# Kernel optimization log

Hardware: AMD Instinct MI355X
Metric: run time of the kernel (lower is better)

The kernel has to match this reference:

```python
import jax, jax.numpy as jnp
import numpy as np

N_NODES = 100000
N_EDGES = 1600000
IN_DIM = 128
HID_DIM = 128
OUT_DIM = 16
N_GRAPHS = 128


def setup_inputs() -> dict:
    key = jax.random.key(0)
    ks = jax.random.split(key, 8)
    x = jax.random.normal(ks[0], (N_NODES, IN_DIM), dtype=jnp.float32)
    edge_index = jax.random.randint(ks[1], (2, N_EDGES), 0, N_NODES, dtype=jnp.int64)
    batch = jnp.sort(jax.random.randint(ks[2], (N_NODES,), 0, N_GRAPHS, dtype=jnp.int64))
    # GCNConv params (glorot-ish scale) and Linear params
    w1 = jax.random.normal(ks[3], (IN_DIM, HID_DIM), dtype=jnp.float32) / np.sqrt(IN_DIM)
    b1 = jnp.zeros((HID_DIM,), dtype=jnp.float32)
    w2 = jax.random.normal(ks[4], (HID_DIM, HID_DIM), dtype=jnp.float32) / np.sqrt(HID_DIM)
    b2 = jnp.zeros((HID_DIM,), dtype=jnp.float32)
    wc = jax.random.normal(ks[5], (HID_DIM, OUT_DIM), dtype=jnp.float32) / np.sqrt(HID_DIM)
    bc = jnp.zeros((OUT_DIM,), dtype=jnp.float32)
    return {"x": x, "edge_index": edge_index, "batch": batch,
            "w1": w1, "b1": b1, "w2": w2, "b2": b2, "wc": wc, "bc": bc}


def _gcn_layer(h, src, dst, w, b, n_nodes):
    # h: [N, Fin]; src/dst: [E+N] (self-loops already appended)
    h = h @ w  # [N, Fout]
    ones = jnp.ones_like(dst, dtype=h.dtype)
    deg = jax.ops.segment_sum(ones, dst, num_segments=n_nodes)  # [N]
    dinv = jnp.where(deg > 0, jax.lax.rsqrt(deg), 0.0)
    norm = dinv[src] * dinv[dst]  # [E+N]
    msg = h[src] * norm[:, None]  # gather + scale, [E+N, Fout]
    out = jax.ops.segment_sum(msg, dst, num_segments=n_nodes)  # scatter-add
    return out + b


def reference(x, edge_index, batch, w1, b1, w2, b2, wc, bc):
    n = x.shape[0]
    loop = jnp.arange(n, dtype=edge_index.dtype)
    src = jnp.concatenate([edge_index[0], loop])  # add self-loops (PyG default)
    dst = jnp.concatenate([edge_index[1], loop])

    h = jax.nn.relu(_gcn_layer(x, src, dst, w1, b1, n))
    h = jax.nn.relu(_gcn_layer(h, src, dst, w2, b2, n))

    # global mean pool over graphs
    sums = jax.ops.segment_sum(h, batch, num_segments=N_GRAPHS)  # [G, H]
    cnt = jax.ops.segment_sum(jnp.ones((n,), h.dtype), batch, num_segments=N_GRAPHS)
    pooled = sums / jnp.maximum(cnt, 1.0)[:, None]

    return pooled @ wc + bc  # [G, OUT_DIM]
```

## Files before the change

kernel.cpp:

```cpp
#include <hip/hip_runtime.h>
#include <stdint.h>

#define NN 100000
#define NE 1600000
#define FDIM 128
#define NGRAPH 128
#define ODIM 16
#define NBKT 391
#define CAP 4608
#define SCHUNK 8192
#define NSCAT ((NE + SCHUNK - 1) / SCHUNK)
#define NSTARTB ((NN + 255) / 256)

typedef __attribute__((ext_vector_type(8))) short short8;
typedef __attribute__((ext_vector_type(8))) unsigned short ushort8;
typedef __attribute__((ext_vector_type(4))) float f32x4;

__device__ __forceinline__ float blo(unsigned int p) { return __uint_as_float(p << 16); }
__device__ __forceinline__ float bhi(unsigned int p) { return __uint_as_float(p & 0xffff0000u); }
__device__ __forceinline__ unsigned short f2b(float f) {
    unsigned int u = __float_as_uint(f);
    unsigned int r = (u + 0x7fffu + ((u >> 16) & 1u)) >> 16;
    return (unsigned short)r;
}
__device__ __forceinline__ unsigned int packbf(float lo, float hi) {
    return (unsigned int)f2b(lo) | ((unsigned int)f2b(hi) << 16);
}

__device__ __forceinline__ int detect_w(const int* __restrict__ ei) {
    int lane = threadIdx.x & 63;
    int v = ei[2 * lane + 1];
    return (__ballot(v != 0) == 0ULL) ? 1 : 0;
}
__device__ __forceinline__ int ld_idx(const int* __restrict__ p, long long i, int w) {
    return w ? p[2 * i] : p[i];
}

__global__ void __launch_bounds__(256) k_prep(
    const float* __restrict__ w1, const float* __restrict__ w2,
    unsigned short* __restrict__ wt1, unsigned short* __restrict__ wt2,
    const int* __restrict__ ei, const int* __restrict__ batch,
    int* __restrict__ gstart, int* __restrict__ bcursor,
    unsigned short* __restrict__ xws)
{
    int b = blockIdx.x, t = threadIdx.x;
    if (b < 128) {
        int idx = b * 256 + t;
        int which = idx >> 14, r = idx & 16383;
        int k = r >> 7, j = r & 127;
        const float* w = which ? w2 : w1;
        unsigned short* wt = which ? wt2 : wt1;
        wt[j * 128 + k] = f2b(w[k * 128 + j]);
    } else if (b < 128 + NSTARTB) {
        int w = detect_w(ei);
        int i = (b - 128) * 256 + t;
        if (i < NN) {
            int bb = ld_idx(batch, i, w);
            int prev = (i == 0) ? -1 : ld_idx(batch, i - 1, w);
            for (int g = prev + 1; g <= bb; ++g) gstart[g] = i;
            if (i == NN - 1)
                for (int g = bb + 1; g <= NGRAPH; ++g) gstart[g] = NN;
        }
    } else {
        int i = (b - 128 - NSTARTB) * 256 + t;
        if (i < NBKT) bcursor[i] = i * CAP;
        if (b == 128 + NSTARTB && t < FDIM) xws[(size_t)NN * FDIM + t] = 0;
    }
}

__global__ void __launch_bounds__(512) k_scat(const int* __restrict__ ei,
                                              int* __restrict__ bcursor,
                                              unsigned int* __restrict__ rec) {
    __shared__ int hist[NBKT];
    __shared__ int gbase[NBKT];
    __shared__ int lcur[NBKT];
    int t = threadIdx.x;
    int w = detect_w(ei);
    for (int i = t; i < NBKT; i += 512) hist[i] = 0;
    __syncthreads();
    long long e0 = (long long)blockIdx.x * SCHUNK;
    unsigned int myrec[16];
    int mybkt[16];
    #pragma unroll
    for (int j = 0; j < 16; ++j) {
        long long e = e0 + j * 512 + t;
        if (e < NE) {
            int s = ld_idx(ei, e, w);
            int d = ld_idx(ei, NE + e, w);
            mybkt[j] = d >> 8;
            myrec[j] = (unsigned int)s | ((unsigned int)(d & 255) << 17);
            atomicAdd(&hist[mybkt[j]], 1);
        } else mybkt[j] = -1;
    }
    __syncthreads();
    for (int i = t; i < NBKT; i += 512) {
        int c = hist[i];
        gbase[i] = c ? atomicAdd(&bcursor[i], c) : 0;
        lcur[i] = 0;
    }
    __syncthreads();
    #pragma unroll
    for (int j = 0; j < 16; ++j) {
        int b = mybkt[j];
        if (b >= 0) {
            int r = atomicAdd(&lcur[b], 1);
            int p = gbase[b] + r;
            if (p < (b + 1) * CAP) rec[p] = myrec[j];
        }
    }
}

__global__ void __launch_bounds__(256) k_bucket(const unsigned int* __restrict__ rec,
                                                const int* __restrict__ bcursor,
                                                int* __restrict__ csr,
                                                int* __restrict__ offs,
                                                int* __restrict__ deg,
                                                float* __restrict__ dinv) {
    __shared__ unsigned int rbuf[CAP];
    __shared__ int srcout[CAP];
    __shared__ int hist[256], scn[256], cur[256];
    int b = blockIdx.x, t = threadIdx.x;
    int base = b * CAP;
    int cnt = bcursor[b] - base;
    if (cnt > CAP) cnt = CAP;
    hist[t] = 0;
    __syncthreads();
    for (int j = t; j < cnt; j += 256) {
        unsigned int r = rec[base + j];
        rbuf[j] = r;
        atomicAdd(&hist[r >> 17], 1);
    }
    __syncthreads();
    int v = hist[t];
    scn[t] = v;
    __syncthreads();
    for (int o = 1; o < 256; o <<= 1) {
        int tv = (t >= o) ? scn[t - o] : 0;
        __syncthreads();
        scn[t] += tv;
        __syncthreads();
    }
    int excl = scn[t] - v;
    cur[t] = excl;
    int node = (b << 8) + t;
    if (node < NN) {
        offs[node] = base + excl;
        deg[node] = v;
        dinv[node] = rsqrtf((float)(v + 1));
    }
    __syncthreads();
    for (int j = t; j < cnt; j += 256) {
        unsigned int r = rbuf[j];
        int p = atomicAdd(&cur[r >> 17], 1);
        srcout[p] = (int)(r & 0x1FFFFu);
    }
    __syncthreads();
    for (int j = t; j < cnt; j += 256) csr[base + j] = srcout[j];
}

#define LWS 136
template <bool BF16IN>
__global__ void __launch_bounds__(256) k_gemm(
    const void* __restrict__ Xv,
    const unsigned short* __restrict__ WT,
    const float* __restrict__ dinv,
    unsigned short* __restrict__ OUT)
{
    __shared__ unsigned short lw[128 * LWS];
    int tid = threadIdx.x;
    for (int it = 0; it < 8; ++it) {
        int vidx = it * 256 + tid;
        int j = vidx >> 4, kc = vidx & 15;
        ushort8 v = *(const ushort8*)(WT + j * 128 + kc * 8);
        *(ushort8*)(&lw[j * LWS + kc * 8]) = v;
    }
    __syncthreads();

    int wave = tid >> 6, lane = tid & 63;
    int quad = lane >> 4, n16 = lane & 15;
    int row0 = (blockIdx.x * 4 + wave) * 16;
    if (row0 >= NN) return;

    f32x4 acc[8];
    for (int ct = 0; ct < 8; ++ct) acc[ct] = (f32x4){0.f, 0.f, 0.f, 0.f};

    const int arow = row0 + n16;
    for (int kk = 0; kk < 4; ++kk) {
        short8 a;
        if (BF16IN) {
            a = *(const short8*)((const unsigned short*)Xv + (size_t)arow * 128 + kk * 32 + quad * 8);
        } else {
            const float* ap = (const float*)Xv + (size_t)arow * 128 + kk * 32 + quad * 8;
            float4 a01 = *(const float4*)(ap);
            float4 a23 = *(const float4*)(ap + 4);
            a[0] = (short)f2b(a01.x); a[1] = (short)f2b(a01.y);
            a[2] = (short)f2b(a01.z); a[3] = (short)f2b(a01.w);
            a[4] = (short)f2b(a23.x); a[5] = (short)f2b(a23.y);
            a[6] = (short)f2b(a23.z); a[7] = (short)f2b(a23.w);
        }
        for (int ct = 0; ct < 8; ++ct) {
            short8 b = *(const short8*)(&lw[(ct * 16 + n16) * LWS + kk * 32 + quad * 8]);
            acc[ct] = __builtin_amdgcn_mfma_f32_16x16x32_bf16(a, b, acc[ct], 0, 0, 0);
        }
    }
    for (int r = 0; r < 4; ++r) {
        int row = row0 + quad * 4 + r;
        float dv = dinv[row];
        for (int ct = 0; ct < 8; ++ct)
            OUT[(size_t)row * 128 + ct * 16 + n16] = f2b(acc[ct][r] * dv);
    }
}

__global__ void __launch_bounds__(256) k_agg(
    const unsigned short* __restrict__ XWS,
    const int* __restrict__ csr,
    const int* __restrict__ offs,
    const int* __restrict__ deg,
    const float* __restrict__ dinv,
    const float* __restrict__ bias,
    unsigned short* __restrict__ H)
{
    int wave = threadIdx.x >> 6, lane = threadIdx.x & 63;
    int v = blockIdx.x * 4 + wave;
    int g = lane >> 4, f = lane & 15;
    int beg = offs[v], end = beg + deg[v];
    float a[8];
    {
        uint4 q = *(const uint4*)(XWS + (size_t)v * FDIM + f * 8);
        float m = (g == 0) ? 1.f : 0.f;
        a[0] = m * blo(q.x); a[1] = m * bhi(q.x); a[2] = m * blo(q.y); a[3] = m * bhi(q.y);
        a[4] = m * blo(q.z); a[5] = m * bhi(q.z); a[6] = m * blo(q.w); a[7] = m * bhi(q.w);
    }
    int e1 = end - 1;
    for (int j = beg; j < end; j += 16) {
        int j0 = j + g, j1 = j + 4 + g, j2 = j + 8 + g, j3 = j + 12 + g;
        int i0 = csr[j0 < end ? j0 : e1]; i0 = (j0 < end) ? i0 : NN;
        int i1 = csr[j1 < end ? j1 : e1]; i1 = (j1 < end) ? i1 : NN;
        int i2 = csr[j2 < end ? j2 : e1]; i2 = (j2 < end) ? i2 : NN;
        int i3 = csr[j3 < end ? j3 : e1]; i3 = (j3 < end) ? i3 : NN;
        uint4 q0 = *(const uint4*)(XWS + (size_t)i0 * FDIM + f * 8);
        uint4 q1 = *(const uint4*)(XWS + (size_t)i1 * FDIM + f * 8);
        uint4 q2 = *(const uint4*)(XWS + (size_t)i2 * FDIM + f * 8);
        uint4 q3 = *(const uint4*)(XWS + (size_t)i3 * FDIM + f * 8);
        a[0] += blo(q0.x); a[1] += bhi(q0.x); a[2] += blo(q0.y); a[3] += bhi(q0.y);
        a[4] += blo(q0.z); a[5] += bhi(q0.z); a[6] += blo(q0.w); a[7] += bhi(q0.w);
        a[0] += blo(q1.x); a[1] += bhi(q1.x); a[2] += blo(q1.y); a[3] += bhi(q1.y);
        a[4] += blo(q1.z); a[5] += bhi(q1.z); a[6] += blo(q1.w); a[7] += bhi(q1.w);
        a[0] += blo(q2.x); a[1] += bhi(q2.x); a[2] += blo(q2.y); a[3] += bhi(q2.y);
        a[4] += blo(q2.z); a[5] += bhi(q2.z); a[6] += blo(q2.w); a[7] += bhi(q2.w);
        a[0] += blo(q3.x); a[1] += bhi(q3.x); a[2] += blo(q3.y); a[3] += bhi(q3.y);
        a[4] += blo(q3.z); a[5] += bhi(q3.z); a[6] += blo(q3.w); a[7] += bhi(q3.w);
    }
    #pragma unroll
    for (int i = 0; i < 8; ++i) {
        a[i] += __shfl_xor(a[i], 16);
        a[i] += __shfl_xor(a[i], 32);
    }
    if (g == 0) {
        float dv = dinv[v];
        float4 b0 = *(const float4*)(bias + f * 8);
        float4 b1 = *(const float4*)(bias + f * 8 + 4);
        uint4 o;
        o.x = packbf(fmaxf(fmaf(a[0], dv, b0.x), 0.f), fmaxf(fmaf(a[1], dv, b0.y), 0.f));
        o.y = packbf(fmaxf(fmaf(a[2], dv, b0.z), 0.f), fmaxf(fmaf(a[3], dv, b0.w), 0.f));
        o.z = packbf(fmaxf(fmaf(a[4], dv, b1.x), 0.f), fmaxf(fmaf(a[5], dv, b1.y), 0.f));
        o.w = packbf(fmaxf(fmaf(a[6], dv, b1.z), 0.f), fmaxf(fmaf(a[7], dv, b1.w), 0.f));
        *(uint4*)(H + (size_t)v * FDIM + f * 8) = o;
    }
}

__global__ void __launch_bounds__(256) k_poolcls(
    const unsigned short* __restrict__ H, const int* __restrict__ gstart,
    const float* __restrict__ wc, const float* __restrict__ bc,
    float* __restrict__ out)
{
    __shared__ float red[512];
    __shared__ float pl[FDIM];
    int g = blockIdx.x;
    int t = threadIdx.x;
    int pair = t & 63;
    int seg = t >> 6;
    int beg = gstart[g], end = gstart[g + 1];
    float a0 = 0.f, a1 = 0.f;
    for (int i = beg + seg; i < end; i += 4) {
        unsigned int q = *(const unsigned int*)(H + (size_t)i * FDIM + 2 * pair);
        a0 += blo(q); a1 += bhi(q);
    }
    red[t] = a0; red[256 + t] = a1;
    __syncthreads();
    if (seg == 0) {
        a0 = red[t] + red[t + 64] + red[t + 128] + red[t + 192];
        a1 = red[256 + t] + red[256 + t + 64] + red[256 + t + 128] + red[256 + t + 192];
        float inv = 1.f / fmaxf((float)(end - beg), 1.f);
        pl[2 * pair] = a0 * inv;
        pl[2 * pair + 1] = a1 * inv;
    }
    __syncthreads();
    int o = t & 15, fs = t >> 4;
    float acc = 0.f;
    #pragma unroll
    for (int k = 0; k < 8; ++k)
        acc += pl[fs * 8 + k] * wc[(fs * 8 + k) * ODIM + o];
    red[t] = acc;
    __syncthreads();
    if (t < 16) {
        float s = bc[t];
        #pragma unroll
        for (int k = 0; k < 16; ++k) s += red[k * 16 + t];
        out[g * ODIM + t] = s;
    }
}

extern "C" void kernel_launch(void* const* d_in, const int* in_sizes, int n_in,
                              void* d_out, int out_size, void* d_ws, size_t ws_size,
                              hipStream_t stream) {
    const float* x   = (const float*)d_in[0];
    const int* ei    = (const int*)d_in[1];
    const int* batch = (const int*)d_in[2];
    const float* w1  = (const float*)d_in[3];
    const float* b1  = (const float*)d_in[4];
    const float* w2  = (const float*)d_in[5];
    const float* b2  = (const float*)d_in[6];
    const float* wc  = (const float*)d_in[7];
    const float* bc  = (const float*)d_in[8];
    float* out = (float*)d_out;

    char* ws = (char*)d_ws;
    size_t off = 0;
    auto alloc = [&](size_t bytes) -> void* {
        off = (off + 255) & ~(size_t)255;
        void* p = ws + off;
        off += bytes;
        return p;
    };
    int*   bcursor = (int*)alloc(NBKT * 4);
    int*   offs    = (int*)alloc(NN * 4);
    int*   deg     = (int*)alloc(NN * 4);
    float* dinv    = (float*)alloc(NN * 4);
    int*   gstart  = (int*)alloc((NGRAPH + 1) * 4);
    unsigned int* rec = (unsigned int*)alloc((size_t)NBKT * CAP * 4);
    int*   csr     = (int*)alloc((size_t)NBKT * CAP * 4 + 256);
    unsigned short* wt1 = (unsigned short*)alloc(128 * 128 * 2);
    unsigned short* wt2 = (unsigned short*)alloc(128 * 128 * 2);
    unsigned short* xws = (unsigned short*)alloc((size_t)(NN + 1) * FDIM * 2);
    unsigned short* h   = (unsigned short*)alloc((size_t)NN * FDIM * 2);

    k_prep<<<128 + NSTARTB + 2, 256, 0, stream>>>(w1, w2, wt1, wt2, ei, batch, gstart, bcursor, xws);
    k_scat<<<NSCAT, 512, 0, stream>>>(ei, bcursor, rec);
    k_bucket<<<NBKT, 256, 0, stream>>>(rec, bcursor, csr, offs, deg, dinv);

    k_gemm<false><<<(NN / 16 + 3) / 4, 256, 0, stream>>>(x, wt1, dinv, xws);
    k_agg<<<NN / 4, 256, 0, stream>>>(xws, csr, offs, deg, dinv, b1, h);
    k_gemm<true><<<(NN / 16 + 3) / 4, 256, 0, stream>>>(h, wt2, dinv, xws);
    k_agg<<<NN / 4, 256, 0, stream>>>(xws, csr, offs, deg, dinv, b2, h);
    k_poolcls<<<NGRAPH, 256, 0, stream>>>(h, gstart, wc, bc, out);
}
```

Baseline: 334.7 us.

## Fuse first-layer aggregation with second-layer GEMM into one kernel

Adds k_aggmm, which aggregates neighbor features for 16 nodes per block, applies bias, ReLU and dinv, stages the bf16 hidden rows in LDS, and multiplies them by W2 with MFMA before writing the scaled result. This removes the second k_gemm launch and the round trip of the hidden activation through global memory. In exchange each block loads the full W2 tile into LDS, and each wave serially aggregates 4 nodes, which lowers parallelism in the gather phase. k_prep is also launched a second time so the new xws2 buffer gets its padding row initialised.

```diff
diff --git a/kernel.cpp b/kernel.cpp
--- a/kernel.cpp
+++ b/kernel.cpp
@@ -159,9 +159,8 @@
 }
 
 #define LWS 136
-template <bool BF16IN>
 __global__ void __launch_bounds__(256) k_gemm(
-    const void* __restrict__ Xv,
+    const float* __restrict__ X,
     const unsigned short* __restrict__ WT,
     const float* __restrict__ dinv,
     unsigned short* __restrict__ OUT)
@@ -186,18 +185,14 @@
 
     const int arow = row0 + n16;
     for (int kk = 0; kk < 4; ++kk) {
+        const float* ap = X + (size_t)arow * 128 + kk * 32 + quad * 8;
+        float4 a01 = *(const float4*)(ap);
+        float4 a23 = *(const float4*)(ap + 4);
         short8 a;
-        if (BF16IN) {
-            a = *(const short8*)((const unsigned short*)Xv + (size_t)arow * 128 + kk * 32 + quad * 8);
-        } else {
-            const float* ap = (const float*)Xv + (size_t)arow * 128 + kk * 32 + quad * 8;
-            float4 a01 = *(const float4*)(ap);
-            float4 a23 = *(const float4*)(ap + 4);
-            a[0] = (short)f2b(a01.x); a[1] = (short)f2b(a01.y);
-            a[2] = (short)f2b(a01.z); a[3] = (short)f2b(a01.w);
-            a[4] = (short)f2b(a23.x); a[5] = (short)f2b(a23.y);
-            a[6] = (short)f2b(a23.z); a[7] = (short)f2b(a23.w);
-        }
+        a[0] = (short)f2b(a01.x); a[1] = (short)f2b(a01.y);
+        a[2] = (short)f2b(a01.z); a[3] = (short)f2b(a01.w);
+        a[4] = (short)f2b(a23.x); a[5] = (short)f2b(a23.y);
+        a[6] = (short)f2b(a23.z); a[7] = (short)f2b(a23.w);
         for (int ct = 0; ct < 8; ++ct) {
             short8 b = *(const short8*)(&lw[(ct * 16 + n16) * LWS + kk * 32 + quad * 8]);
             acc[ct] = __builtin_amdgcn_mfma_f32_16x16x32_bf16(a, b, acc[ct], 0, 0, 0);
@@ -208,6 +203,97 @@
         float dv = dinv[row];
         for (int ct = 0; ct < 8; ++ct)
             OUT[(size_t)row * 128 + ct * 16 + n16] = f2b(acc[ct][r] * dv);
+    }
+}
+
+__global__ void __launch_bounds__(256) k_aggmm(
+    const unsigned short* __restrict__ XWS,
+    const unsigned short* __restrict__ WT2,
+    const int* __restrict__ csr,
+    const int* __restrict__ offs,
+    const int* __restrict__ deg,
+    const float* __restrict__ dinv,
+    const float* __restrict__ bias,
+    unsigned short* __restrict__ OUT)
+{
+    __shared__ unsigned short lw[128 * LWS];
+    __shared__ unsigned short lh[16 * LWS];
+    int tid = threadIdx.x;
+    for (int it = 0; it < 8; ++it) {
+        int vidx = it * 256 + tid;
+        int j = vidx >> 4, kc = vidx & 15;
+        ushort8 v = *(const ushort8*)(WT2 + j * 128 + kc * 8);
+        *(ushort8*)(&lw[j * LWS + kc * 8]) = v;
+    }
+    int wave = tid >> 6, lane = tid & 63;
+    int g = lane >> 4, f = lane & 15;
+    int n0 = blockIdx.x * 16;
+
+    for (int nn = 0; nn < 4; ++nn) {
+        int v = n0 + wave * 4 + nn;
+        int beg = offs[v], end = beg + deg[v];
+        float a[8];
+        {
+            uint4 q = *(const uint4*)(XWS + (size_t)v * FDIM + f * 8);
+            float m = (g == 0) ? 1.f : 0.f;
+            a[0] = m * blo(q.x); a[1] = m * bhi(q.x); a[2] = m * blo(q.y); a[3] = m * bhi(q.y);
+            a[4] = m * blo(q.z); a[5] = m * bhi(q.z); a[6] = m * blo(q.w); a[7] = m * bhi(q.w);
+        }
+        int e1 = end - 1;
+        for (int j = beg; j < end; j += 16) {
+            int j0 = j + g, j1 = j + 4 + g, j2 = j + 8 + g, j3 = j + 12 + g;
+            int i0 = csr[j0 < end ? j0 : e1]; i0 = (j0 < end) ? i0 : NN;
+            int i1 = csr[j1 < end ? j1 : e1]; i1 = (j1 < end) ? i1 : NN;
+            int i2 = csr[j2 < end ? j2 : e1]; i2 = (j2 < end) ? i2 : NN;
+            int i3 = csr[j3 < end ? j3 : e1]; i3 = (j3 < end) ? i3 : NN;
+            uint4 q0 = *(const uint4*)(XWS + (size_t)i0 * FDIM + f * 8);
+            uint4 q1 = *(const uint4*)(XWS + (size_t)i1 * FDIM + f * 8);
+            uint4 q2 = *(const uint4*)(XWS + (size_t)i2 * FDIM + f * 8);
+            uint4 q3 = *(const uint4*)(XWS + (size_t)i3 * FDIM + f * 8);
+            a[0] += blo(q0.x); a[1] += bhi(q0.x); a[2] += blo(q0.y); a[3] += bhi(q0.y);
+            a[4] += blo(q0.z); a[5] += bhi(q0.z); a[6] += blo(q0.w); a[7] += bhi(q0.w);
+            a[0] += blo(q1.x); a[1] += bhi(q1.x); a[2] += blo(q1.y); a[3] += bhi(q1.y);
+            a[4] += blo(q1.z); a[5] += bhi(q1.z); a[6] += blo(q1.w); a[7] += bhi(q1.w);
+            a[0] += blo(q2.x); a[1] += bhi(q2.x); a[2] += blo(q2.y); a[3] += bhi(q2.y);
+            a[4] += blo(q2.z); a[5] += bhi(q2.z); a[6] += blo(q2.w); a[7] += bhi(q2.w);
+            a[0] += blo(q3.x); a[1] += bhi(q3.x); a[2] += blo(q3.y); a[3] += bhi(q3.y);
+            a[4] += blo(q3.z); a[5] += bhi(q3.z); a[6] += blo(q3.w); a[7] += bhi(q3.w);
+        }
+        #pragma unroll
+        for (int i = 0; i < 8; ++i) {
+            a[i] += __shfl_xor(a[i], 16);
+            a[i] += __shfl_xor(a[i], 32);
+        }
+        if (g == 0) {
+            float dv = dinv[v];
+            float4 b0 = *(const float4*)(bias + f * 8);
+            float4 b1 = *(const float4*)(bias + f * 8 + 4);
+            uint4 o;
+            o.x = packbf(fmaxf(fmaf(a[0], dv, b0.x), 0.f), fmaxf(fmaf(a[1], dv, b0.y), 0.f));
+            o.y = packbf(fmaxf(fmaf(a[2], dv, b0.z), 0.f), fmaxf(fmaf(a[3], dv, b0.w), 0.f));
+            o.z = packbf(fmaxf(fmaf(a[4], dv, b1.x), 0.f), fmaxf(fmaf(a[5], dv, b1.y), 0.f));
+            o.w = packbf(fmaxf(fmaf(a[6], dv, b1.z), 0.f), fmaxf(fmaf(a[7], dv, b1.w), 0.f));
+            *(uint4*)(&lh[(wave * 4 + nn) * LWS + f * 8]) = o;
+        }
+    }
+    __syncthreads();
+
+    int quad = lane >> 4, n16 = lane & 15;
+    f32x4 acc0 = (f32x4){0.f, 0.f, 0.f, 0.f};
+    f32x4 acc1 = (f32x4){0.f, 0.f, 0.f, 0.f};
+    int ct0 = wave * 2, ct1 = wave * 2 + 1;
+    for (int kk = 0; kk < 4; ++kk) {
+        short8 a = *(const short8*)(&lh[n16 * LWS + kk * 32 + quad * 8]);
+        short8 b0 = *(const short8*)(&lw[(ct0 * 16 + n16) * LWS + kk * 32 + quad * 8]);
+        short8 b1 = *(const short8*)(&lw[(ct1 * 16 + n16) * LWS + kk * 32 + quad * 8]);
+        acc0 = __builtin_amdgcn_mfma_f32_16x16x32_bf16(a, b0, acc0, 0, 0, 0);
+        acc1 = __builtin_amdgcn_mfma_f32_16x16x32_bf16(a, b1, acc1, 0, 0, 0);
+    }
+    for (int r = 0; r < 4; ++r) {
+        int row = n0 + quad * 4 + r;
+        float dv = dinv[row];
+        OUT[(size_t)row * 128 + ct0 * 16 + n16] = f2b(acc0[r] * dv);
+        OUT[(size_t)row * 128 + ct1 * 16 + n16] = f2b(acc1[r] * dv);
     }
 }
 
@@ -342,16 +428,17 @@
     int*   csr     = (int*)alloc((size_t)NBKT * CAP * 4 + 256);
     unsigned short* wt1 = (unsigned short*)alloc(128 * 128 * 2);
     unsigned short* wt2 = (unsigned short*)alloc(128 * 128 * 2);
-    unsigned short* xws = (unsigned short*)alloc((size_t)(NN + 1) * FDIM * 2);
-    unsigned short* h   = (unsigned short*)alloc((size_t)NN * FDIM * 2);
+    unsigned short* xws  = (unsigned short*)alloc((size_t)(NN + 1) * FDIM * 2);
+    unsigned short* xws2 = (unsigned short*)alloc((size_t)(NN + 1) * FDIM * 2);
+    unsigned short* h2   = (unsigned short*)alloc((size_t)NN * FDIM * 2);
 
     k_prep<<<128 + NSTARTB + 2, 256, 0, stream>>>(w1, w2, wt1, wt2, ei, batch, gstart, bcursor, xws);
+    k_prep<<<128 + NSTARTB + 2, 256, 0, stream>>>(w1, w2, wt1, wt2, ei, batch, gstart, bcursor, xws2);
     k_scat<<<NSCAT, 512, 0, stream>>>(ei, bcursor, rec);
     k_bucket<<<NBKT, 256, 0, stream>>>(rec, bcursor, csr, offs, deg, dinv);
 
-    k_gemm<false><<<(NN / 16 + 3) / 4, 256, 0, stream>>>(x, wt1, dinv, xws);
-    k_agg<<<NN / 4, 256, 0, stream>>>(xws, csr, offs, deg, dinv, b1, h);
-    k_gemm<true><<<(NN / 16 + 3) / 4, 256, 0, stream>>>(h, wt2, dinv, xws);
-    k_agg<<<NN / 4, 256, 0, stream>>>(xws, csr, offs, deg, dinv, b2, h);
-    k_poolcls<<<NGRAPH, 256, 0, stream>>>(h, gstart, wc, bc, out);
-}
+    k_gemm<<<(NN / 16 + 3) / 4, 256, 0, stream>>>(x, wt1, dinv, xws);
+    k_aggmm<<<NN / 16, 256, 0, stream>>>(xws, wt2, csr, offs, deg, dinv, b1, xws2);
+    k_agg<<<NN / 4, 256, 0, stream>>>(xws2, csr, offs, deg, dinv, b2, h2);
+    k_poolcls<<<NGRAPH, 256, 0, stream>>>(h2, gstart, wc, bc, out);
+}
```

After: 349.4 us. 4.4% more time.
